# Kernel optimization log

Hardware: AMD Instinct MI355X
Metric: run time of the kernel (lower is better)

## Reference

```python
import jax, jax.numpy as jnp
import numpy as np

NEG_INF = -9e15
ALPHA = 0.2  # LeakyReLU negative slope


def setup_inputs() -> dict:
    key = jax.random.key(0)
    k1, k2, k3, k4 = jax.random.split(key, 4)
    B, N, C_IN, C_OUT, H = 8, 2048, 256, 256, 4
    node_feats = jax.random.normal(k1, (B, N, C_IN), dtype=jnp.float32)
    adj_matrix = jax.random.randint(k2, (B, N, N), 0, 2, dtype=jnp.int32)
    # include self-connections as the docstring expects
    eye = jnp.eye(N, dtype=jnp.int32)[None]
    adj_matrix = jnp.maximum(adj_matrix, eye)
    W = jax.random.normal(k3, (C_OUT, C_IN), dtype=jnp.float32) * (1.414 / np.sqrt(C_IN))
    b = jnp.zeros((C_OUT,), dtype=jnp.float32)
    a = jax.random.normal(k4, (H, 2 * (C_OUT // H)), dtype=jnp.float32) * 0.1
    return {"node_feats": node_feats, "adj_matrix": adj_matrix, "W": W, "b": b, "a": a}


def reference(node_feats, adj_matrix, W, b, a):
    B, N, _ = node_feats.shape
    H, two_c = a.shape
    c = two_c // 2
    # projection: [B, N, H, c]
    f = (jnp.einsum('bni,oi->bno', node_feats, W) + b).reshape(B, N, H, c)
    # attention logit for edge (i, j): leakyrelu(a . [f_i, f_j])
    # decomposes as leakyrelu(s_src[i] + s_dst[j])
    a_src, a_dst = a[:, :c], a[:, c:]
    s_src = jnp.einsum('bnhc,hc->bnh', f, a_src)  # [B, N, H]
    s_dst = jnp.einsum('bnhc,hc->bnh', f, a_dst)  # [B, N, H]
    logits = jax.nn.leaky_relu(s_src[:, :, None, :] + s_dst[:, None, :, :], ALPHA)  # [B,N,N,H]
    logits = jnp.where(adj_matrix[..., None] == 1, logits, NEG_INF)
    probs = jax.nn.softmax(logits, axis=2)  # softmax over source nodes j
    out = jnp.einsum('bijh,bjhc->bihc', probs, f)
    return out.reshape(B, N, H * c)  # concat_heads=True
```

## Files before the change

### kernel.cpp

```cpp
#include <hip/hip_runtime.h>

#define LOG2E 1.4426950408889634f

typedef __attribute__((ext_vector_type(8))) short short8;
typedef __attribute__((ext_vector_type(16))) float f32x16;

__device__ __forceinline__ unsigned short f2bf(float f) {
  unsigned int u = __float_as_uint(f);
  u = (u + 0x7fffu + ((u >> 16) & 1u)) >> 16;
  return (unsigned short)u;
}

__global__ __launch_bounds__(256) void gat_k1(
    const float* __restrict__ X, const float* __restrict__ W,
    const float* __restrict__ bias, const float* __restrict__ a,
    unsigned short* __restrict__ ft, float* __restrict__ ssrc,
    float* __restrict__ sdst)
{
  __shared__ float Xs[8][128];
  __shared__ float Ws[8][128];
  const int tid = threadIdx.x;
  const int tx = tid & 15, ty = tid >> 4;
  const int m0 = blockIdx.x * 128;
  const int c0 = blockIdx.y * 128;

  float acc[8][8];
#pragma unroll
  for (int r = 0; r < 8; ++r)
#pragma unroll
    for (int j = 0; j < 8; ++j) acc[r][j] = 0.f;

  const int lrow = tid >> 1;
  const int kk0 = (tid & 1) * 4;
  const float* Xp = X + (size_t)(m0 + lrow) * 256 + kk0;
  const float* Wp = W + (size_t)(c0 + lrow) * 256 + kk0;

  for (int kc = 0; kc < 256; kc += 8) {
    float4 xv = *(const float4*)(Xp + kc);
    float4 wv = *(const float4*)(Wp + kc);
    __syncthreads();
    Xs[kk0 + 0][lrow] = xv.x; Xs[kk0 + 1][lrow] = xv.y;
    Xs[kk0 + 2][lrow] = xv.z; Xs[kk0 + 3][lrow] = xv.w;
    Ws[kk0 + 0][lrow] = wv.x; Ws[kk0 + 1][lrow] = wv.y;
    Ws[kk0 + 2][lrow] = wv.z; Ws[kk0 + 3][lrow] = wv.w;
    __syncthreads();
#pragma unroll
    for (int kk = 0; kk < 8; ++kk) {
      float av[8], wv8[8];
#pragma unroll
      for (int r = 0; r < 8; ++r) av[r] = Xs[kk][ty * 8 + r];
#pragma unroll
      for (int j = 0; j < 8; ++j) wv8[j] = Ws[kk][tx * 8 + j];
#pragma unroll
      for (int r = 0; r < 8; ++r)
#pragma unroll
        for (int j = 0; j < 8; ++j) acc[r][j] = fmaf(av[r], wv8[j], acc[r][j]);
    }
  }

  const int b = m0 >> 11;
  const int nloc0 = (m0 & 2047) + ty * 8;
  const int cg0 = c0 + tx * 8;
  const int h = cg0 >> 6;
  const int cb = cg0 & 63;

  float bv[8], av_s[8], av_d[8];
#pragma unroll
  for (int j = 0; j < 8; ++j) {
    bv[j]   = bias[cg0 + j];
    av_s[j] = a[h * 128 + cb + j];
    av_d[j] = a[h * 128 + 64 + cb + j];
  }
#pragma unroll
  for (int r = 0; r < 8; ++r)
#pragma unroll
    for (int j = 0; j < 8; ++j) acc[r][j] += bv[j];

  const int jt = nloc0 >> 4;
  const int ni = nloc0 & 15;
#pragma unroll
  for (int j = 0; j < 8; ++j) {
    unsigned int u[4];
#pragma unroll
    for (int q = 0; q < 4; ++q) {
      unsigned int lo = f2bf(acc[2 * q + 0][j]);
      unsigned int hi = f2bf(acc[2 * q + 1][j]);
      u[q] = lo | (hi << 16);
    }
    size_t off = ((((size_t)b * 128 + jt) * 4 + h) * 64 + (cb + j)) * 16 + ni;
    *(uint4*)(ft + off) = make_uint4(u[0], u[1], u[2], u[3]);
  }

  float sp[8], dp[8];
#pragma unroll
  for (int r = 0; r < 8; ++r) {
    float s = 0.f, d = 0.f;
#pragma unroll
    for (int j = 0; j < 8; ++j) {
      s = fmaf(acc[r][j], av_s[j], s);
      d = fmaf(acc[r][j], av_d[j], d);
    }
    sp[r] = s; dp[r] = d;
  }
#pragma unroll
  for (int off = 1; off < 8; off <<= 1) {
#pragma unroll
    for (int r = 0; r < 8; ++r) {
      sp[r] += __shfl_xor(sp[r], off);
      dp[r] += __shfl_xor(dp[r], off);
    }
  }
  if ((tx & 7) == 0) {
    float* sb = ssrc + ((size_t)b * 4 + h) * 2048 + nloc0;
    float* db = sdst + ((size_t)b * 4 + h) * 2048 + nloc0;
#pragma unroll
    for (int r = 0; r < 8; ++r) { sb[r] = sp[r] * LOG2E; db[r] = dp[r] * LOG2E; }
  }
}

__global__ __launch_bounds__(512, 4) void gat_k2(
    const int* __restrict__ adj, const unsigned short* __restrict__ ft,
    const float* __restrict__ ssrc, const float* __restrict__ sdst,
    float* __restrict__ out)
{
  __shared__ __align__(16) unsigned char lds[33280];
  float* sd = (float*)lds;

  const int tid = threadIdx.x;
  const int b = blockIdx.x & 7;
  const int itile = blockIdx.x >> 3;
  const int i0 = itile * 32;
  const int w = tid >> 6;
  const int h = w >> 1;
  const int p = w & 1;
  const int lane = tid & 63;
  const int l31 = lane & 31;
  const int kh = lane >> 5;

  {
    const float4* src = (const float4*)(sdst + (size_t)b * 4 * 2048);
    float4* dst = (float4*)sd;
#pragma unroll
    for (int q = 0; q < 4; ++q) dst[tid + q * 512] = src[tid + q * 512];
  }
  const float si = ssrc[((size_t)b * 4 + h) * 2048 + i0 + l31];

  const unsigned short* ftb =
      ft + ((((size_t)b * 128 + p) * 4 + h) * 64 + l31) * 16 + kh * 8;
  const int* adjp = adj + (size_t)b * 2048 * 2048 +
                    (size_t)(i0 + l31) * 2048 + p * 16 + kh * 8;
  const float* sdh = sd + h * 2048 + p * 16 + kh * 8;

  f32x16 acc0, acc1;
#pragma unroll
  for (int q = 0; q < 16; ++q) { acc0[q] = 0.f; acc1[q] = 0.f; }
  float lsum = 0.f;

  __syncthreads();

  struct Pref { uint4 fb0, fb1; int4 a0, a1; };

  auto LOADS = [&](int s, Pref& P) {
    const unsigned short* fp = ftb + (size_t)s * 8192;
    P.fb0 = *(const uint4*)fp;
    P.fb1 = *(const uint4*)(fp + 512);
    const int* ap = adjp + s * 32;
    P.a0 = *(const int4*)ap;
    P.a1 = *(const int4*)(ap + 4);
  };

  auto COMP = [&](int s, const Pref& P) {
    const float* tp = sdh + s * 32;
    float4 t0 = *(const float4*)tp;
    float4 t1 = *(const float4*)(tp + 4);
    float tj[8] = {t0.x, t0.y, t0.z, t0.w, t1.x, t1.y, t1.z, t1.w};
    int ai[8] = {P.a0.x, P.a0.y, P.a0.z, P.a0.w, P.a1.x, P.a1.y, P.a1.z, P.a1.w};
    float e[8];
#pragma unroll
    for (int q = 0; q < 8; ++q) {
      float x = si + tj[q];
      float y = fmaxf(x, 0.2f * x);
      float ev = __builtin_amdgcn_exp2f(y);
      ev = ai[q] ? ev : 0.f;
      e[q] = ev;
      lsum += ev;
    }
    union { unsigned u[4]; short8 v; } af;
#pragma unroll
    for (int q2 = 0; q2 < 4; ++q2) {
      unsigned r;
      asm("v_cvt_pk_bf16_f32 %0, %1, %2" : "=v"(r) : "v"(e[2 * q2]), "v"(e[2 * q2 + 1]));
      af.u[q2] = r;
    }
    union { uint4 q; short8 v; } b0, b1;
    b0.q = P.fb0; b1.q = P.fb1;
    acc0 = __builtin_amdgcn_mfma_f32_32x32x16_bf16(af.v, b0.v, acc0, 0, 0, 0);
    acc1 = __builtin_amdgcn_mfma_f32_32x32x16_bf16(af.v, b1.v, acc1, 0, 0, 0);
  };

  Pref A, B;
  LOADS(0, A);
  for (int s = 0; s < 62; s += 2) {
    LOADS(s + 1, B);
    COMP(s, A);
    LOADS(s + 2, A);
    COMP(s + 1, B);
  }
  LOADS(63, B);
  COMP(62, A);
  COMP(63, B);

  float lsum2 = lsum + __shfl_xor(lsum, 32);
  float* ep = (float*)lds;
  float* el = (float*)(lds + 32768);
  __syncthreads();
  if (p == 1) {
#pragma unroll
    for (int reg = 0; reg < 16; ++reg) {
      const int row = (reg & 3) + 8 * (reg >> 2) + 4 * kh;
      ep[(h * 32 + row) * 64 + l31]      = acc0[reg];
      ep[(h * 32 + row) * 64 + l31 + 32] = acc1[reg];
    }
    if (lane < 32) el[h * 32 + l31] = lsum2;
  }
  __syncthreads();
  if (p == 0) {
    const float L = lsum2 + el[h * 32 + l31];
    const float rinv = 1.0f / L;
    float* ob = out + ((size_t)(b * 2048 + i0)) * 256 + h * 64;
#pragma unroll
    for (int reg = 0; reg < 16; ++reg) {
      const int row = (reg & 3) + 8 * (reg >> 2) + 4 * kh;
      const float ri = __shfl(rinv, row);
      const float o0 = (acc0[reg] + ep[(h * 32 + row) * 64 + l31]) * ri;
      const float o1 = (acc1[reg] + ep[(h * 32 + row) * 64 + l31 + 32]) * ri;
      ob[(size_t)row * 256 + l31]      = o0;
      ob[(size_t)row * 256 + l31 + 32] = o1;
    }
  }
}

extern "C" void kernel_launch(void* const* d_in, const int* in_sizes, int n_in,
                              void* d_out, int out_size, void* d_ws, size_t ws_size,
                              hipStream_t stream) {
  const float* X    = (const float*)d_in[0];
  const int*   adj  = (const int*)d_in[1];
  const float* W    = (const float*)d_in[2];
  const float* bias = (const float*)d_in[3];
  const float* a    = (const float*)d_in[4];
  float* out = (float*)d_out;

  unsigned short* ft = (unsigned short*)d_ws;
  float* ssrc = (float*)((char*)d_ws + 8388608);
  float* sdst = ssrc + 8 * 4 * 2048;

  gat_k1<<<dim3(128, 2, 1), 256, 0, stream>>>(X, W, bias, a, ft, ssrc, sdst);
  gat_k2<<<dim3(512, 1, 1), 512, 0, stream>>>(adj, ft, ssrc, sdst, out);
}
```

Before: 125.4 us.

## Pack adjacency into bitmask inside projection kernel and deepen ft prefetch

Extra blocks in the projection kernel read the int32 adjacency matrix and pack it into 64-bit ballot masks in workspace. The attention kernel then stages a per-tile bitmask into LDS instead of streaming 32-bit adjacency entries inside its MFMA loop. The feature prefetch is also deepened from two to four stages. The adjacency is still read once in full, now concurrently with the GEMM, and this adds an extra workspace write and read plus LDS usage.

```diff
diff --git a/kernel.cpp b/kernel.cpp
--- a/kernel.cpp
+++ b/kernel.cpp
@@ -14,15 +14,29 @@
 __global__ __launch_bounds__(256) void gat_k1(
     const float* __restrict__ X, const float* __restrict__ W,
     const float* __restrict__ bias, const float* __restrict__ a,
+    const int* __restrict__ adj,
     unsigned short* __restrict__ ft, float* __restrict__ ssrc,
-    float* __restrict__ sdst)
+    float* __restrict__ sdst, unsigned long long* __restrict__ bits)
 {
+  if (blockIdx.x >= 256) {
+    const int pb = blockIdx.x - 256;
+    const int gw = (pb << 2) + (threadIdx.x >> 6);
+    const int lane = threadIdx.x & 63;
+    for (int c = gw; c < 524288; c += 8192) {
+      const size_t base = ((size_t)c) << 6;
+      int v = adj[base + lane];
+      unsigned long long m = __ballot(v != 0);
+      if (lane == 0) bits[c] = m;
+    }
+    return;
+  }
+
   __shared__ float Xs[8][128];
   __shared__ float Ws[8][128];
   const int tid = threadIdx.x;
   const int tx = tid & 15, ty = tid >> 4;
-  const int m0 = blockIdx.x * 128;
-  const int c0 = blockIdx.y * 128;
+  const int m0 = (blockIdx.x >> 1) * 128;
+  const int c0 = (blockIdx.x & 1) * 128;
 
   float acc[8][8];
 #pragma unroll
@@ -119,12 +133,13 @@
 }
 
 __global__ __launch_bounds__(512, 4) void gat_k2(
-    const int* __restrict__ adj, const unsigned short* __restrict__ ft,
+    const void* __restrict__ bitsv, const unsigned short* __restrict__ ft,
     const float* __restrict__ ssrc, const float* __restrict__ sdst,
     float* __restrict__ out)
 {
-  __shared__ __align__(16) unsigned char lds[33280];
+  __shared__ __align__(16) unsigned char lds[41216];
   float* sd = (float*)lds;
+  unsigned* Aw = (unsigned*)(lds + 32768);
 
   const int tid = threadIdx.x;
   const int b = blockIdx.x & 7;
@@ -136,6 +151,7 @@
   const int lane = tid & 63;
   const int l31 = lane & 31;
   const int kh = lane >> 5;
+  const int shamt = (2 * p + kh) * 8;
 
   {
     const float4* src = (const float4*)(sdst + (size_t)b * 4 * 2048);
@@ -143,12 +159,20 @@
 #pragma unroll
     for (int q = 0; q < 4; ++q) dst[tid + q * 512] = src[tid + q * 512];
   }
+  {
+    const uint4* bsrc = (const uint4*)((const char*)bitsv +
+                                       ((size_t)(b * 2048 + i0)) * 256);
+    uint4 v = bsrc[tid];
+    const int row = tid >> 4, w0 = (tid & 15) * 4;
+    Aw[(w0 + 0) * 33 + row] = v.x;
+    Aw[(w0 + 1) * 33 + row] = v.y;
+    Aw[(w0 + 2) * 33 + row] = v.z;
+    Aw[(w0 + 3) * 33 + row] = v.w;
+  }
   const float si = ssrc[((size_t)b * 4 + h) * 2048 + i0 + l31];
 
   const unsigned short* ftb =
       ft + ((((size_t)b * 128 + p) * 4 + h) * 64 + l31) * 16 + kh * 8;
-  const int* adjp = adj + (size_t)b * 2048 * 2048 +
-                    (size_t)(i0 + l31) * 2048 + p * 16 + kh * 8;
   const float* sdh = sd + h * 2048 + p * 16 + kh * 8;
 
   f32x16 acc0, acc1;
@@ -158,57 +182,65 @@
 
   __syncthreads();
 
-  struct Pref { uint4 fb0, fb1; int4 a0, a1; };
-
-  auto LOADS = [&](int s, Pref& P) {
-    const unsigned short* fp = ftb + (size_t)s * 8192;
-    P.fb0 = *(const uint4*)fp;
-    P.fb1 = *(const uint4*)(fp + 512);
-    const int* ap = adjp + s * 32;
-    P.a0 = *(const int4*)ap;
-    P.a1 = *(const int4*)(ap + 4);
-  };
-
-  auto COMP = [&](int s, const Pref& P) {
-    const float* tp = sdh + s * 32;
-    float4 t0 = *(const float4*)tp;
-    float4 t1 = *(const float4*)(tp + 4);
-    float tj[8] = {t0.x, t0.y, t0.z, t0.w, t1.x, t1.y, t1.z, t1.w};
-    int ai[8] = {P.a0.x, P.a0.y, P.a0.z, P.a0.w, P.a1.x, P.a1.y, P.a1.z, P.a1.w};
-    float e[8];
-#pragma unroll
-    for (int q = 0; q < 8; ++q) {
-      float x = si + tj[q];
-      float y = fmaxf(x, 0.2f * x);
-      float ev = __builtin_amdgcn_exp2f(y);
-      ev = ai[q] ? ev : 0.f;
-      e[q] = ev;
-      lsum += ev;
-    }
-    union { unsigned u[4]; short8 v; } af;
-#pragma unroll
-    for (int q2 = 0; q2 < 4; ++q2) {
-      unsigned r;
-      asm("v_cvt_pk_bf16_f32 %0, %1, %2" : "=v"(r) : "v"(e[2 * q2]), "v"(e[2 * q2 + 1]));
-      af.u[q2] = r;
-    }
-    union { uint4 q; short8 v; } b0, b1;
-    b0.q = P.fb0; b1.q = P.fb1;
-    acc0 = __builtin_amdgcn_mfma_f32_32x32x16_bf16(af.v, b0.v, acc0, 0, 0, 0);
-    acc1 = __builtin_amdgcn_mfma_f32_32x32x16_bf16(af.v, b1.v, acc1, 0, 0, 0);
-  };
-
-  Pref A, B;
-  LOADS(0, A);
-  for (int s = 0; s < 62; s += 2) {
-    LOADS(s + 1, B);
-    COMP(s, A);
-    LOADS(s + 2, A);
-    COMP(s + 1, B);
-  }
-  LOADS(63, B);
-  COMP(62, A);
-  COMP(63, B);
+  uint4 f0a, f0b, f1a, f1b, f2a, f2b, f3a, f3b;
+
+#define LOADF(s, fa, fb)                                          \
+  {                                                               \
+    const unsigned short* fp_ = ftb + (size_t)(s) * 8192;         \
+    fa = *(const uint4*)fp_;                                      \
+    fb = *(const uint4*)(fp_ + 512);                              \
+  }
+
+#define COMP(s, fa, fb)                                           \
+  {                                                               \
+    const unsigned wrd = Aw[(s) * 33 + l31];                      \
+    const unsigned byte_ = (wrd >> shamt) & 0xffu;                \
+    const float* tp_ = sdh + (s) * 32;                            \
+    float4 t0_ = *(const float4*)tp_;                             \
+    float4 t1_ = *(const float4*)(tp_ + 4);                       \
+    float tj_[8] = {t0_.x, t0_.y, t0_.z, t0_.w,                   \
+                    t1_.x, t1_.y, t1_.z, t1_.w};                  \
+    float e_[8];                                                  \
+    _Pragma("unroll")                                             \
+    for (int q = 0; q < 8; ++q) {                                 \
+      float x_ = si + tj_[q];                                     \
+      float y_ = fmaxf(x_, 0.2f * x_);                            \
+      float ev_ = __builtin_amdgcn_exp2f(y_);                     \
+      ev_ = (byte_ & (1u << q)) ? ev_ : 0.f;                      \
+      e_[q] = ev_;                                                \
+      lsum += ev_;                                                \
+    }                                                             \
+    union { unsigned u[4]; short8 v; } af_;                       \
+    _Pragma("unroll")                                             \
+    for (int q2 = 0; q2 < 4; ++q2) {                              \
+      unsigned r_;                                                \
+      asm("v_cvt_pk_bf16_f32 %0, %1, %2"                          \
+          : "=v"(r_) : "v"(e_[2 * q2]), "v"(e_[2 * q2 + 1]));     \
+      af_.u[q2] = r_;                                             \
+    }                                                             \
+    union { uint4 q; short8 v; } b0_, b1_;                        \
+    b0_.q = fa; b1_.q = fb;                                       \
+    acc0 = __builtin_amdgcn_mfma_f32_32x32x16_bf16(af_.v, b0_.v, acc0, 0, 0, 0); \
+    acc1 = __builtin_amdgcn_mfma_f32_32x32x16_bf16(af_.v, b1_.v, acc1, 0, 0, 0); \
+  }
+
+  LOADF(0, f0a, f0b)
+  LOADF(1, f1a, f1b)
+  LOADF(2, f2a, f2b)
+  LOADF(3, f3a, f3b)
+
+  for (int s = 0; s < 64; s += 4) {
+    const int n0 = (s + 4 < 64) ? s + 4 : 63;
+    const int n1 = (s + 5 < 64) ? s + 5 : 63;
+    const int n2 = (s + 6 < 64) ? s + 6 : 63;
+    const int n3 = (s + 7 < 64) ? s + 7 : 63;
+    COMP(s + 0, f0a, f0b) LOADF(n0, f0a, f0b)
+    COMP(s + 1, f1a, f1b) LOADF(n1, f1a, f1b)
+    COMP(s + 2, f2a, f2b) LOADF(n2, f2a, f2b)
+    COMP(s + 3, f3a, f3b) LOADF(n3, f3a, f3b)
+  }
+#undef LOADF
+#undef COMP
 
   float lsum2 = lsum + __shfl_xor(lsum, 32);
   float* ep = (float*)lds;
@@ -253,7 +285,10 @@
   unsigned short* ft = (unsigned short*)d_ws;
   float* ssrc = (float*)((char*)d_ws + 8388608);
   float* sdst = ssrc + 8 * 4 * 2048;
-
-  gat_k1<<<dim3(128, 2, 1), 256, 0, stream>>>(X, W, bias, a, ft, ssrc, sdst);
-  gat_k2<<<dim3(512, 1, 1), 512, 0, stream>>>(adj, ft, ssrc, sdst, out);
-}
+  unsigned long long* bits =
+      (unsigned long long*)((char*)d_ws + 8912896);
+
+  gat_k1<<<dim3(2304, 1, 1), 256, 0, stream>>>(X, W, bias, a, adj,
+                                               ft, ssrc, sdst, bits);
+  gat_k2<<<dim3(512, 1, 1), 512, 0, stream>>>(bits, ft, ssrc, sdst, out);
+}
```

Result: slower. 132.0 us (+5.3%).

## Restructure GAT aggregation: bitmask adjacency in LDS, async feature staging, 16x16 MFMA

Applied to the files above, without the earlier changes.

The aggregation kernel now reads the block's 32-row adjacency slab once up front and packs it into 16-bit masks in LDS. Feature tiles are double-buffered into LDS with global_load_lds async copies, and the wave split changes from two K-halves per head to two 16-row groups using 16x16x32 bf16 MFMAs. The softmax denominator comes from an extra MFMA against a ones vector, which removes the cross-wave LDS reduction of partial sums. The cost is a larger LDS footprint (about 74KB) that lowers occupancy, plus a block-wide barrier every K step.

```diff
diff --git a/kernel.cpp b/kernel.cpp
--- a/kernel.cpp
+++ b/kernel.cpp
@@ -2,8 +2,10 @@
 
 #define LOG2E 1.4426950408889634f
 
-typedef __attribute__((ext_vector_type(8))) short short8;
-typedef __attribute__((ext_vector_type(16))) float f32x16;
+typedef __attribute__((ext_vector_type(8))) short bf16x8;
+typedef __attribute__((ext_vector_type(4))) float f32x4;
+
+union AF { unsigned u[4]; bf16x8 v; };
 
 __device__ __forceinline__ unsigned short f2bf(float f) {
   unsigned int u = __float_as_uint(f);
@@ -123,19 +125,40 @@
     const float* __restrict__ ssrc, const float* __restrict__ sdst,
     float* __restrict__ out)
 {
-  __shared__ __align__(16) unsigned char lds[33280];
+  __shared__ __align__(16) unsigned char lds[73984];
   float* sd = (float*)lds;
+  unsigned* Aw = (unsigned*)(lds + 32768);
+  unsigned short* ftl = (unsigned short*)(lds + 41216);
 
   const int tid = threadIdx.x;
   const int b = blockIdx.x & 7;
   const int itile = blockIdx.x >> 3;
   const int i0 = itile * 32;
-  const int w = tid >> 6;
-  const int h = w >> 1;
-  const int p = w & 1;
+  const int wv = tid >> 6;
+  const int h = wv >> 1;
+  const int rg = wv & 1;
   const int lane = tid & 63;
-  const int l31 = lane & 31;
-  const int kh = lane >> 5;
+  const int i_l = lane & 15;
+  const int kg = lane >> 4;
+  const int shamt = kg * 8;
+
+  const char* ftg = (const char*)ft + (size_t)b * 1048576 +
+                    wv * 2048 + (lane << 4);
+
+#define STAGE(s_, buf_)                                                     \
+  {                                                                         \
+    const char* g_ = ftg + (size_t)(s_) * 16384;                            \
+    __builtin_amdgcn_global_load_lds(                                       \
+        (const __attribute__((address_space(1))) unsigned int*)g_,          \
+        (__attribute__((address_space(3))) unsigned int*)(ftl +             \
+            (buf_) * 8192 + wv * 1024), 16, 0, 0);                          \
+    __builtin_amdgcn_global_load_lds(                                       \
+        (const __attribute__((address_space(1))) unsigned int*)(g_ + 1024), \
+        (__attribute__((address_space(3))) unsigned int*)(ftl +             \
+            (buf_) * 8192 + wv * 1024 + 512), 16, 0, 0);                    \
+  }
+
+  STAGE(0, 0)
 
   {
     const float4* src = (const float4*)(sdst + (size_t)b * 4 * 2048);
@@ -143,100 +166,90 @@
 #pragma unroll
     for (int q = 0; q < 4; ++q) dst[tid + q * 512] = src[tid + q * 512];
   }
-  const float si = ssrc[((size_t)b * 4 + h) * 2048 + i0 + l31];
-
-  const unsigned short* ftb =
-      ft + ((((size_t)b * 128 + p) * 4 + h) * 64 + l31) * 16 + kh * 8;
-  const int* adjp = adj + (size_t)b * 2048 * 2048 +
-                    (size_t)(i0 + l31) * 2048 + p * 16 + kh * 8;
-  const float* sdh = sd + h * 2048 + p * 16 + kh * 8;
-
-  f32x16 acc0, acc1;
-#pragma unroll
-  for (int q = 0; q < 16; ++q) { acc0[q] = 0.f; acc1[q] = 0.f; }
-  float lsum = 0.f;
+  {
+    const int* abase = adj + (size_t)b * 4194304 + (size_t)i0 * 2048;
+    unsigned short* dst16 = (unsigned short*)Aw;
+#pragma unroll
+    for (int k = 0; k < 8; ++k) {
+      const int idx = k * 512 + tid;
+      const int r = idx >> 7;
+      const int s16 = idx & 127;
+      const int4* ap = (const int4*)(abase + (size_t)r * 2048 + s16 * 16);
+      int4 v0 = ap[0], v1 = ap[1], v2 = ap[2], v3 = ap[3];
+      int vv[16] = {v0.x, v0.y, v0.z, v0.w, v1.x, v1.y, v1.z, v1.w,
+                    v2.x, v2.y, v2.z, v2.w, v3.x, v3.y, v3.z, v3.w};
+      unsigned m = 0;
+#pragma unroll
+      for (int i = 0; i < 16; ++i) m |= (vv[i] ? 1u : 0u) << i;
+      dst16[((s16 >> 1) * 33 + r) * 2 + (s16 & 1)] = (unsigned short)m;
+    }
+  }
+  const float si = ssrc[((size_t)b * 4 + h) * 2048 + i0 + rg * 16 + i_l];
+  const float* sdh = sd + h * 2048 + kg * 8;
+  const unsigned* awp = Aw + rg * 16 + i_l;
+
+  f32x4 acc0, acc1, acc2, acc3, acc4;
+#pragma unroll
+  for (int q = 0; q < 4; ++q) {
+    acc0[q] = 0.f; acc1[q] = 0.f; acc2[q] = 0.f; acc3[q] = 0.f; acc4[q] = 0.f;
+  }
+  bf16x8 ones;
+#pragma unroll
+  for (int q = 0; q < 8; ++q) ones[q] = (short)0x3F80;
 
   __syncthreads();
 
-  struct Pref { uint4 fb0, fb1; int4 a0, a1; };
-
-  auto LOADS = [&](int s, Pref& P) {
-    const unsigned short* fp = ftb + (size_t)s * 8192;
-    P.fb0 = *(const uint4*)fp;
-    P.fb1 = *(const uint4*)(fp + 512);
-    const int* ap = adjp + s * 32;
-    P.a0 = *(const int4*)ap;
-    P.a1 = *(const int4*)(ap + 4);
-  };
-
-  auto COMP = [&](int s, const Pref& P) {
+  const int fbase = (kg >> 1) * 4096 + h * 1024 + i_l * 16 + (kg & 1) * 8;
+
+  for (int s = 0; s < 64; ++s) {
+    if (s < 63) STAGE(s + 1, (s + 1) & 1)
+
+    const unsigned mw = awp[s * 33];
     const float* tp = sdh + s * 32;
     float4 t0 = *(const float4*)tp;
     float4 t1 = *(const float4*)(tp + 4);
+    const unsigned byte_ = (mw >> shamt) & 0xffu;
     float tj[8] = {t0.x, t0.y, t0.z, t0.w, t1.x, t1.y, t1.z, t1.w};
-    int ai[8] = {P.a0.x, P.a0.y, P.a0.z, P.a0.w, P.a1.x, P.a1.y, P.a1.z, P.a1.w};
     float e[8];
 #pragma unroll
     for (int q = 0; q < 8; ++q) {
       float x = si + tj[q];
       float y = fmaxf(x, 0.2f * x);
       float ev = __builtin_amdgcn_exp2f(y);
-      ev = ai[q] ? ev : 0.f;
-      e[q] = ev;
-      lsum += ev;
-    }
-    union { unsigned u[4]; short8 v; } af;
+      e[q] = (byte_ & (1u << q)) ? ev : 0.f;
+    }
+    AF af;
 #pragma unroll
     for (int q2 = 0; q2 < 4; ++q2) {
-      unsigned r;
-      asm("v_cvt_pk_bf16_f32 %0, %1, %2" : "=v"(r) : "v"(e[2 * q2]), "v"(e[2 * q2 + 1]));
-      af.u[q2] = r;
-    }
-    union { uint4 q; short8 v; } b0, b1;
-    b0.q = P.fb0; b1.q = P.fb1;
-    acc0 = __builtin_amdgcn_mfma_f32_32x32x16_bf16(af.v, b0.v, acc0, 0, 0, 0);
-    acc1 = __builtin_amdgcn_mfma_f32_32x32x16_bf16(af.v, b1.v, acc1, 0, 0, 0);
-  };
-
-  Pref A, B;
-  LOADS(0, A);
-  for (int s = 0; s < 62; s += 2) {
-    LOADS(s + 1, B);
-    COMP(s, A);
-    LOADS(s + 2, A);
-    COMP(s + 1, B);
-  }
-  LOADS(63, B);
-  COMP(62, A);
-  COMP(63, B);
-
-  float lsum2 = lsum + __shfl_xor(lsum, 32);
-  float* ep = (float*)lds;
-  float* el = (float*)(lds + 32768);
-  __syncthreads();
-  if (p == 1) {
-#pragma unroll
-    for (int reg = 0; reg < 16; ++reg) {
-      const int row = (reg & 3) + 8 * (reg >> 2) + 4 * kh;
-      ep[(h * 32 + row) * 64 + l31]      = acc0[reg];
-      ep[(h * 32 + row) * 64 + l31 + 32] = acc1[reg];
-    }
-    if (lane < 32) el[h * 32 + l31] = lsum2;
-  }
-  __syncthreads();
-  if (p == 0) {
-    const float L = lsum2 + el[h * 32 + l31];
-    const float rinv = 1.0f / L;
-    float* ob = out + ((size_t)(b * 2048 + i0)) * 256 + h * 64;
-#pragma unroll
-    for (int reg = 0; reg < 16; ++reg) {
-      const int row = (reg & 3) + 8 * (reg >> 2) + 4 * kh;
-      const float ri = __shfl(rinv, row);
-      const float o0 = (acc0[reg] + ep[(h * 32 + row) * 64 + l31]) * ri;
-      const float o1 = (acc1[reg] + ep[(h * 32 + row) * 64 + l31 + 32]) * ri;
-      ob[(size_t)row * 256 + l31]      = o0;
-      ob[(size_t)row * 256 + l31 + 32] = o1;
-    }
+      unsigned r_;
+      asm("v_cvt_pk_bf16_f32 %0, %1, %2"
+          : "=v"(r_) : "v"(e[2 * q2]), "v"(e[2 * q2 + 1]));
+      af.u[q2] = r_;
+    }
+    const unsigned short* fb = ftl + (s & 1) * 8192 + fbase;
+    bf16x8 F0 = *(const bf16x8*)(fb);
+    bf16x8 F1 = *(const bf16x8*)(fb + 256);
+    bf16x8 F2 = *(const bf16x8*)(fb + 512);
+    bf16x8 F3 = *(const bf16x8*)(fb + 768);
+    acc0 = __builtin_amdgcn_mfma_f32_16x16x32_bf16(af.v, F0, acc0, 0, 0, 0);
+    acc1 = __builtin_amdgcn_mfma_f32_16x16x32_bf16(af.v, F1, acc1, 0, 0, 0);
+    acc2 = __builtin_amdgcn_mfma_f32_16x16x32_bf16(af.v, F2, acc2, 0, 0, 0);
+    acc3 = __builtin_amdgcn_mfma_f32_16x16x32_bf16(af.v, F3, acc3, 0, 0, 0);
+    acc4 = __builtin_amdgcn_mfma_f32_16x16x32_bf16(af.v, ones, acc4, 0, 0, 0);
+
+    __syncthreads();
+  }
+#undef STAGE
+
+  float* ob = out + ((size_t)(b * 2048 + i0 + rg * 16)) * 256 + h * 64;
+#pragma unroll
+  for (int r = 0; r < 4; ++r) {
+    const int row = kg * 4 + r;
+    const float ri = 1.0f / acc4[r];
+    ob[(size_t)row * 256 + 0  + i_l] = acc0[r] * ri;
+    ob[(size_t)row * 256 + 16 + i_l] = acc1[r] * ri;
+    ob[(size_t)row * 256 + 32 + i_l] = acc2[r] * ri;
+    ob[(size_t)row * 256 + 48 + i_l] = acc3[r] * ri;
   }
 }
 
```

Measured after the change: 116.7 us. 1.07x faster.
